# Kernel tuning notes

Hardware: AMD Instinct MI355X
Metric: run time of the kernel (lower is better)

Reference implementation:

```python
import jax, jax.numpy as jnp
import numpy as np

DIM = 768
NUM_HEADS = 12
HEAD_DIM = DIM // NUM_HEADS
SCALE = HEAD_DIM ** -0.5


def setup_inputs() -> dict:
    key = jax.random.key(0)
    k_x, k_qkv, k_proj, k_pb = jax.random.split(key, 4)
    B, N, C = 16, 1024, DIM
    x = jax.random.normal(k_x, (B, N, C), dtype=jnp.float32)
    # qkv Linear: weight [3C, C], no bias (qkv_bias=False)
    w_qkv = jax.random.normal(k_qkv, (3 * C, C), dtype=jnp.float32) * (C ** -0.5)
    # proj Linear: weight [C, C], bias [C]
    w_proj = jax.random.normal(k_proj, (C, C), dtype=jnp.float32) * (C ** -0.5)
    b_proj = jax.random.normal(k_pb, (C,), dtype=jnp.float32) * 0.01
    return {"x": x, "w_qkv": w_qkv, "w_proj": w_proj, "b_proj": b_proj}


def reference(x, w_qkv, w_proj, b_proj):
    B, N, C = x.shape
    H, D = NUM_HEADS, HEAD_DIM
    # qkv projection: [B,N,3C] -> [3,B,H,N,D]
    qkv = jnp.einsum('bnc,ec->bne', x, w_qkv)
    qkv = qkv.reshape(B, N, 3, H, D).transpose(2, 0, 3, 1, 4)
    q, k, v = qkv[0], qkv[1], qkv[2]
    # manual attention: scores [B,H,N,N] materialized, as in source
    attn = jnp.einsum('bhqd,bhkd->bhqk', q, k) * SCALE
    attn = jax.nn.softmax(attn, axis=-1)
    out = jnp.einsum('bhqk,bhkd->bhqd', attn, v)  # [B,H,N,D]
    out = out.transpose(0, 2, 1, 3).reshape(B, N, C)
    out = jnp.einsum('bnc,oc->bno', out, w_proj) + b_proj
    return out
```

## Files before the change

kernel.cpp:

```cpp
#include <hip/hip_runtime.h>
#include <hip/hip_bf16.h>
#include <stdint.h>

typedef __attribute__((ext_vector_type(8))) short short8;
typedef __attribute__((ext_vector_type(4))) short short4v;
typedef __attribute__((ext_vector_type(4))) float floatx4;

#define B_   16
#define N_   1024
#define C_   768
#define H_   12
#define D_   64
#define K_   768
#define QSCALE 0.18033688011112042f

__device__ __forceinline__ short f2bf(float f) {
    __hip_bfloat16 h = __float2bfloat16(f);
    short s; __builtin_memcpy(&s, &h, 2); return s;
}
__device__ __forceinline__ unsigned pk2bf(float a, float b) {
    __hip_bfloat162 h = __float22bfloat162_rn(make_float2(a, b));
    unsigned u; __builtin_memcpy(&u, &h, 4); return u;
}

__device__ __forceinline__ void gl_lds16(const void* g, void* l) {
    __builtin_amdgcn_global_load_lds(
        (const __attribute__((address_space(1))) unsigned int*)g,
        (__attribute__((address_space(3))) unsigned int*)l, 16, 0, 0);
}

#define N8_X  1572864
#define N8_WQ 221184
#define N8_WP 73728
__global__ void cvt_all(const float* __restrict__ x, const float* __restrict__ wq,
                        const float* __restrict__ wp, short* __restrict__ xb,
                        short* __restrict__ wqb, short* __restrict__ wpb)
{
    long i = (long)blockIdx.x * 256 + threadIdx.x;
    const float* src; short* dst;
    if (i < N8_X)              { src = x;  dst = xb;  }
    else if (i < N8_X + N8_WQ) { src = wq; dst = wqb; i -= N8_X; }
    else                       { src = wp; dst = wpb; i -= (long)N8_X + N8_WQ; }
    const float4* p = (const float4*)src + 2 * i;
    const float4 u = p[0], v = p[1];
    short8 r;
    r[0] = f2bf(u.x); r[1] = f2bf(u.y); r[2] = f2bf(u.z); r[3] = f2bf(u.w);
    r[4] = f2bf(v.x); r[5] = f2bf(v.y); r[6] = f2bf(v.z); r[7] = f2bf(v.w);
    *((short8*)dst + i) = r;
}

template<int MODE>
__global__ __launch_bounds__(256, 3)
void gemm_bt(const short* __restrict__ A, const short* __restrict__ Bm,
             const float* __restrict__ bias,
             short* __restrict__ q_ws, short* __restrict__ k_ws,
             short* __restrict__ v_ws, float* __restrict__ outp)
{
    __shared__ short Alds[128 * 32];
    __shared__ short Blds[128 * 32];
    const int tid  = threadIdx.x;
    const int wave = tid >> 6, lane = tid & 63;
    const int cl   = lane & 15, quad = lane >> 4;
    const int bm = blockIdx.x, bn = blockIdx.y;
    const int wm = (wave >> 1) * 64, wn = (wave & 1) * 64;

    const short* Ag = A  + (long)bm * 128 * K_ + (long)(tid >> 2) * K_ + (tid & 3) * 8;
    const short* Bg = Bm + (long)bn * 128 * K_ + (long)(tid >> 2) * K_ + (tid & 3) * 8;
    short* la = Alds + (tid & 0xC0) * 8;
    short* lb = Blds + (tid & 0xC0) * 8;

    const floatx4 fzero = {0.f, 0.f, 0.f, 0.f};
    floatx4 acc[4][4];
    #pragma unroll
    for (int i = 0; i < 4; i++)
        #pragma unroll
        for (int j = 0; j < 4; j++) acc[i][j] = fzero;

    for (int kt = 0; kt < K_; kt += 32) {
        __syncthreads();
        gl_lds16(Ag + kt,            la);
        gl_lds16(Ag + kt + 64 * K_,  la + 2048);
        gl_lds16(Bg + kt,            lb);
        gl_lds16(Bg + kt + 64 * K_,  lb + 2048);
        __syncthreads();

        short8 af[4], bf[4];
        #pragma unroll
        for (int i = 0; i < 4; i++)
            af[i] = *(const short8*)(Alds + (wm + i * 16 + cl) * 32 + quad * 8);
        #pragma unroll
        for (int j = 0; j < 4; j++)
            bf[j] = *(const short8*)(Blds + (wn + j * 16 + cl) * 32 + quad * 8);
        #pragma unroll
        for (int i = 0; i < 4; i++)
            #pragma unroll
            for (int j = 0; j < 4; j++)
                acc[i][j] = __builtin_amdgcn_mfma_f32_16x16x32_bf16(af[i], bf[j], acc[i][j], 0, 0, 0);
    }

    #pragma unroll
    for (int i = 0; i < 4; i++) {
        const int gm0 = bm * 128 + wm + i * 16 + quad * 4;
        #pragma unroll
        for (int j = 0; j < 4; j++) {
            const int gn = bn * 128 + wn + j * 16 + cl;
            if (MODE == 0) {
                const int t   = bn / 6;
                const int rem = gn - t * 768;
                const int h   = rem >> 6, d = rem & 63;
                const int b   = gm0 >> 10;
                const int n0  = gm0 & 1023;
                const int bh  = b * H_ + h;
                if (t == 2) {
                    short4v pk;
                    #pragma unroll
                    for (int r = 0; r < 4; r++) pk[r] = f2bf(acc[i][j][r]);
                    *(short4v*)(v_ws + (((long)(bh * D_ + d)) << 10) + n0) = pk;
                } else {
                    short* dst = (t == 0) ? q_ws : k_ws;
                    const float sc = (t == 0) ? QSCALE : 1.0f;
                    #pragma unroll
                    for (int r = 0; r < 4; r++)
                        dst[((long)bh * N_ + (n0 + r)) * D_ + d] = f2bf(acc[i][j][r] * sc);
                }
            } else {
                const float bv = bias[gn];
                #pragma unroll
                for (int r = 0; r < 4; r++)
                    outp[(long)(gm0 + r) * C_ + gn] = acc[i][j][r] + bv;
            }
        }
    }
}

#define PSTRIDE (16 * 72 + 3072)
__global__ __launch_bounds__(256, 3)
void attn_fused(const short* __restrict__ q_ws, const short* __restrict__ k_ws,
                const short* __restrict__ v_ws, short* __restrict__ o_ws)
{
    __shared__ short Klds[64 * 64];
    __shared__ short Vlds[64 * 64];
    __shared__ short Plds[4 * PSTRIDE];

    const int tid  = threadIdx.x;
    const int wave = tid >> 6, lane = tid & 63;
    const int cl   = lane & 15, quad = lane >> 4;

    const int linear = blockIdx.y * 8 + blockIdx.x;
    const int xcd = linear & 7, slot = linear >> 3;
    const int bh  = xcd * 24 + (slot >> 3);
    const int qt  = slot & 7;

    const long base = (long)bh * (N_ * D_);
    const int  qr0  = qt * 128 + wave * 32 + cl;

    short8 qf[2][2];
    #pragma unroll
    for (int mt = 0; mt < 2; mt++) {
        qf[mt][0] = *(const short8*)(q_ws + base + (long)(qr0 + mt * 16) * D_ + quad * 8);
        qf[mt][1] = *(const short8*)(q_ws + base + (long)(qr0 + mt * 16) * D_ + 32 + quad * 8);
    }

    const floatx4 fzero = {0.f, 0.f, 0.f, 0.f};
    float m_r[2][4], l_r[2][4];
    floatx4 o_acc[2][4];
    #pragma unroll
    for (int mt = 0; mt < 2; mt++)
        #pragma unroll
        for (int r = 0; r < 4; r++) {
            m_r[mt][r] = -1e30f; l_r[mt][r] = 0.f; o_acc[mt][r] = fzero;
        }

    const int srow = tid >> 2;
    const int sg0  = (tid & 3) * 2;
    const int xw   = srow & 7;
    short* pl = &Plds[wave * PSTRIDE];

    for (int kc = 0; kc < N_; kc += 64) {
        short8 k0 = *(const short8*)(k_ws + base + (long)(kc + srow) * D_ + sg0 * 8);
        short8 k1 = *(const short8*)(k_ws + base + (long)(kc + srow) * D_ + sg0 * 8 + 8);
        short8 v0 = *(const short8*)(v_ws + base + (long)srow * N_ + kc + sg0 * 8);
        short8 v1 = *(const short8*)(v_ws + base + (long)srow * N_ + kc + sg0 * 8 + 8);
        __syncthreads();
        *(short8*)(Klds + srow * 64 + ((sg0    ) ^ xw) * 8) = k0;
        *(short8*)(Klds + srow * 64 + ((sg0 + 1) ^ xw) * 8) = k1;
        *(short8*)(Vlds + srow * 64 + ((sg0    ) ^ xw) * 8) = v0;
        *(short8*)(Vlds + srow * 64 + ((sg0 + 1) ^ xw) * 8) = v1;
        __syncthreads();

        #pragma unroll
        for (int mt = 0; mt < 2; mt++) {
            floatx4 s[4];
            #pragma unroll
            for (int nt = 0; nt < 4; nt++) {
                const int krow = cl * 4 + nt;
                const int xr   = krow & 7;
                const short* kr = Klds + krow * 64;
                short8 kf0 = *(const short8*)(kr + ((quad    ) ^ xr) * 8);
                short8 kf1 = *(const short8*)(kr + ((quad + 4) ^ xr) * 8);
                floatx4 t4 = fzero;
                t4 = __builtin_amdgcn_mfma_f32_16x16x32_bf16(qf[mt][0], kf0, t4, 0, 0, 0);
                t4 = __builtin_amdgcn_mfma_f32_16x16x32_bf16(qf[mt][1], kf1, t4, 0, 0, 0);
                s[nt] = t4;
            }

            float alpha[4];
            #pragma unroll
            for (int r = 0; r < 4; r++) {
                float v = fmaxf(fmaxf(s[0][r], s[1][r]), fmaxf(s[2][r], s[3][r]));
                v = fmaxf(v, __shfl_xor(v, 1));
                v = fmaxf(v, __shfl_xor(v, 2));
                v = fmaxf(v, __shfl_xor(v, 4));
                v = fmaxf(v, __shfl_xor(v, 8));
                const float mn = fmaxf(m_r[mt][r], v);
                alpha[r] = __builtin_amdgcn_exp2f(m_r[mt][r] - mn);
                m_r[mt][r] = mn;
                l_r[mt][r] *= alpha[r];
            }
            #pragma unroll
            for (int r = 0; r < 4; r++) {
                float p0 = __builtin_amdgcn_exp2f(s[0][r] - m_r[mt][r]);
                float p1 = __builtin_amdgcn_exp2f(s[1][r] - m_r[mt][r]);
                float p2 = __builtin_amdgcn_exp2f(s[2][r] - m_r[mt][r]);
                float p3 = __builtin_amdgcn_exp2f(s[3][r] - m_r[mt][r]);
                l_r[mt][r] += (p0 + p1) + (p2 + p3);
                uint2 pk = { pk2bf(p0, p1), pk2bf(p2, p3) };
                *(uint2*)(pl + (quad * 4 + r) * 72 + cl * 4) = pk;
            }
            #pragma unroll
            for (int dt = 0; dt < 4; dt++) {
                o_acc[mt][dt][0] *= alpha[0]; o_acc[mt][dt][1] *= alpha[1];
                o_acc[mt][dt][2] *= alpha[2]; o_acc[mt][dt][3] *= alpha[3];
            }
            asm volatile("" ::: "memory");

            #pragma unroll
            for (int ks = 0; ks < 2; ks++) {
                short8 pf = *(const short8*)(pl + cl * 72 + ks * 32 + quad * 8);
                #pragma unroll
                for (int dt = 0; dt < 4; dt++) {
                    const int vrow = dt * 16 + cl;
                    const int xr   = vrow & 7;
                    const short* vr = Vlds + vrow * 64;
                    short8 vf = *(const short8*)(vr + ((ks * 4 + quad) ^ xr) * 8);
                    o_acc[mt][dt] = __builtin_amdgcn_mfma_f32_16x16x32_bf16(pf, vf, o_acc[mt][dt], 0, 0, 0);
                }
            }
            asm volatile("" ::: "memory");
        }
    }

    const int b = bh / H_, h = bh - b * H_;
    #pragma unroll
    for (int mt = 0; mt < 2; mt++) {
        #pragma unroll
        for (int r = 0; r < 4; r++) {
            float v = l_r[mt][r];
            v += __shfl_xor(v, 1); v += __shfl_xor(v, 2);
            v += __shfl_xor(v, 4); v += __shfl_xor(v, 8);
            l_r[mt][r] = 1.0f / v;
        }
        const int nrow = qt * 128 + wave * 32 + mt * 16 + quad * 4;
        #pragma unroll
        for (int dt = 0; dt < 4; dt++) {
            const int c = h * D_ + dt * 16 + cl;
            #pragma unroll
            for (int r = 0; r < 4; r++)
                o_ws[((long)(b * N_ + nrow + r)) * C_ + c] = f2bf(o_acc[mt][dt][r] * l_r[mt][r]);
        }
    }
}

extern "C" void kernel_launch(void* const* d_in, const int* in_sizes, int n_in,
                              void* d_out, int out_size, void* d_ws, size_t ws_size,
                              hipStream_t stream)
{
    const float* x      = (const float*)d_in[0];
    const float* w_qkv  = (const float*)d_in[1];
    const float* w_proj = (const float*)d_in[2];
    const float* b_proj = (const float*)d_in[3];
    float* out = (float*)d_out;

    const long SZ = (long)B_ * N_ * C_;
    short* q_ws   = (short*)d_ws;
    short* k_ws   = q_ws + SZ;
    short* v_ws   = k_ws + SZ;
    short* x_bf   = v_ws + SZ;
    short* o_ws   = x_bf;
    short* wqkv_bf  = x_bf + SZ;
    short* wproj_bf = wqkv_bf + (long)3 * C_ * C_;

    cvt_all<<<dim3(7296), 256, 0, stream>>>(x, w_qkv, w_proj, x_bf, wqkv_bf, wproj_bf);
    gemm_bt<0><<<dim3(128, 18), 256, 0, stream>>>(x_bf, wqkv_bf, nullptr, q_ws, k_ws, v_ws, nullptr);
    attn_fused<<<dim3(8, 192), 256, 0, stream>>>(q_ws, k_ws, v_ws, o_ws);
    gemm_bt<1><<<dim3(128, 6), 256, 0, stream>>>(o_ws, wproj_bf, b_proj, nullptr, nullptr, nullptr, out);
}
```

Baseline: 337.2 us.

## Double-buffer K/V tiles in attention and change LDS swizzle pattern

The attention kernel now keeps two LDS buffers for K and V. It prefetches the next 64-key tile into registers while computing on the current one, then writes it to the other buffer, so each iteration needs one barrier instead of two. The XOR swizzle changes from row&7 to a function of row>>1 and row>>4, aimed at reducing bank conflicts on the MFMA operand reads. The padded P buffer is also shrunk. Total LDS use changes, which could affect occupancy at 3 blocks/CU, and the prefetched values raise register pressure.

```diff
diff --git a/kernel.cpp b/kernel.cpp
--- a/kernel.cpp
+++ b/kernel.cpp
@@ -28,6 +28,8 @@
         (const __attribute__((address_space(1))) unsigned int*)g,
         (__attribute__((address_space(3))) unsigned int*)l, 16, 0, 0);
 }
+
+#define FSWZ(row) ((((row) >> 1) ^ ((row) >> 4)) & 7)
 
 #define N8_X  1572864
 #define N8_WQ 221184
@@ -133,14 +135,13 @@
     }
 }
 
-#define PSTRIDE (16 * 72 + 3072)
 __global__ __launch_bounds__(256, 3)
 void attn_fused(const short* __restrict__ q_ws, const short* __restrict__ k_ws,
                 const short* __restrict__ v_ws, short* __restrict__ o_ws)
 {
-    __shared__ short Klds[64 * 64];
-    __shared__ short Vlds[64 * 64];
-    __shared__ short Plds[4 * PSTRIDE];
+    __shared__ short Klds[2][64 * 64];
+    __shared__ short Vlds[2][64 * 64];
+    __shared__ short Plds[4][16 * 72];
 
     const int tid  = threadIdx.x;
     const int wave = tid >> 6, lane = tid & 63;
@@ -173,20 +174,33 @@
 
     const int srow = tid >> 2;
     const int sg0  = (tid & 3) * 2;
-    const int xw   = srow & 7;
-    short* pl = &Plds[wave * PSTRIDE];
+    const int xw   = FSWZ(srow);
+    short* pl = &Plds[wave][0];
+
+    {
+        short8 k0 = *(const short8*)(k_ws + base + (long)srow * D_ + sg0 * 8);
+        short8 k1 = *(const short8*)(k_ws + base + (long)srow * D_ + sg0 * 8 + 8);
+        short8 v0 = *(const short8*)(v_ws + base + (long)srow * N_ + sg0 * 8);
+        short8 v1 = *(const short8*)(v_ws + base + (long)srow * N_ + sg0 * 8 + 8);
+        *(short8*)(&Klds[0][0] + srow * 64 + ((sg0    ) ^ xw) * 8) = k0;
+        *(short8*)(&Klds[0][0] + srow * 64 + ((sg0 + 1) ^ xw) * 8) = k1;
+        *(short8*)(&Vlds[0][0] + srow * 64 + ((sg0    ) ^ xw) * 8) = v0;
+        *(short8*)(&Vlds[0][0] + srow * 64 + ((sg0 + 1) ^ xw) * 8) = v1;
+    }
+    __syncthreads();
 
     for (int kc = 0; kc < N_; kc += 64) {
-        short8 k0 = *(const short8*)(k_ws + base + (long)(kc + srow) * D_ + sg0 * 8);
-        short8 k1 = *(const short8*)(k_ws + base + (long)(kc + srow) * D_ + sg0 * 8 + 8);
-        short8 v0 = *(const short8*)(v_ws + base + (long)srow * N_ + kc + sg0 * 8);
-        short8 v1 = *(const short8*)(v_ws + base + (long)srow * N_ + kc + sg0 * 8 + 8);
-        __syncthreads();
-        *(short8*)(Klds + srow * 64 + ((sg0    ) ^ xw) * 8) = k0;
-        *(short8*)(Klds + srow * 64 + ((sg0 + 1) ^ xw) * 8) = k1;
-        *(short8*)(Vlds + srow * 64 + ((sg0    ) ^ xw) * 8) = v0;
-        *(short8*)(Vlds + srow * 64 + ((sg0 + 1) ^ xw) * 8) = v1;
-        __syncthreads();
+        const int cb = (kc >> 6) & 1;
+        const int kn = kc + 64;
+        short8 nk0, nk1, nv0, nv1;
+        if (kn < N_) {
+            nk0 = *(const short8*)(k_ws + base + (long)(kn + srow) * D_ + sg0 * 8);
+            nk1 = *(const short8*)(k_ws + base + (long)(kn + srow) * D_ + sg0 * 8 + 8);
+            nv0 = *(const short8*)(v_ws + base + (long)srow * N_ + kn + sg0 * 8);
+            nv1 = *(const short8*)(v_ws + base + (long)srow * N_ + kn + sg0 * 8 + 8);
+        }
+        const short* Kc = &Klds[cb][0];
+        const short* Vc = &Vlds[cb][0];
 
         #pragma unroll
         for (int mt = 0; mt < 2; mt++) {
@@ -194,8 +208,8 @@
             #pragma unroll
             for (int nt = 0; nt < 4; nt++) {
                 const int krow = cl * 4 + nt;
-                const int xr   = krow & 7;
-                const short* kr = Klds + krow * 64;
+                const int xr   = FSWZ(krow);
+                const short* kr = Kc + krow * 64;
                 short8 kf0 = *(const short8*)(kr + ((quad    ) ^ xr) * 8);
                 short8 kf1 = *(const short8*)(kr + ((quad + 4) ^ xr) * 8);
                 floatx4 t4 = fzero;
@@ -240,14 +254,24 @@
                 #pragma unroll
                 for (int dt = 0; dt < 4; dt++) {
                     const int vrow = dt * 16 + cl;
-                    const int xr   = vrow & 7;
-                    const short* vr = Vlds + vrow * 64;
+                    const int xr   = FSWZ(vrow);
+                    const short* vr = Vc + vrow * 64;
                     short8 vf = *(const short8*)(vr + ((ks * 4 + quad) ^ xr) * 8);
                     o_acc[mt][dt] = __builtin_amdgcn_mfma_f32_16x16x32_bf16(pf, vf, o_acc[mt][dt], 0, 0, 0);
                 }
             }
             asm volatile("" ::: "memory");
         }
+
+        if (kn < N_) {
+            short* Kn = &Klds[cb ^ 1][0];
+            short* Vn = &Vlds[cb ^ 1][0];
+            *(short8*)(Kn + srow * 64 + ((sg0    ) ^ xw) * 8) = nk0;
+            *(short8*)(Kn + srow * 64 + ((sg0 + 1) ^ xw) * 8) = nk1;
+            *(short8*)(Vn + srow * 64 + ((sg0    ) ^ xw) * 8) = nv0;
+            *(short8*)(Vn + srow * 64 + ((sg0 + 1) ^ xw) * 8) = nv1;
+        }
+        __syncthreads();
     }
 
     const int b = bh / H_, h = bh - b * H_;
```

Measured after the change: 345.6 us. 1.02x slower.
